# Kernel optimization log

Hardware: AMD Instinct MI355X
Metric: run time of the kernel (lower is better)

The kernel has to match this reference:

```python
import jax, jax.numpy as jnp
import numpy as np
from jax import lax

TAU_MIN = 0.01
TAU_MAX = 10.0
SLOW_TAU = 5.0


def setup_inputs() -> dict:
    key = jax.random.key(0)
    ks = iter(jax.random.split(key, 40))
    def p(shape, scale=0.05):
        return (jax.random.normal(next(ks), shape, jnp.float32) * scale)
    B, T, D = 1024, 512, 31
    FU, SU, H = 32, 32, 64
    inp = {
        "x": jax.random.normal(next(ks), (B, T, D), jnp.float32),
        # FlashFloodGate: Linear(62->32), Linear(32->1)
        "fg_w1": p((32, 2 * D)), "fg_b1": p((32,)),
        "fg_w2": p((1, 32)), "fg_b2": p((1,)),
        # fast LTC cell
        "fwin": p((FU, D)), "fbin": p((FU,)), "fwrec": p((FU, FU)),
        # slow LTC cell
        "swin": p((SU, D)), "sbin": p((SU,)), "swrec": p((SU, SU)),
        # fusion Linear(64->64)
        "fu_w": p((H, FU + SU)), "fu_b": p((H,)),
        # attention Linear(64->32), Linear(32->1)
        "at_w1": p((32, H)), "at_b1": p((32,)),
        "at_w2": p((1, 32)), "at_b2": p((1,)),
        # depth head Linear(64->64), Linear(64->5)
        "d_w1": p((64, H)), "d_b1": p((64,)),
        "d_w2": p((5, 64)), "d_b2": p((5,)),
        # overflow head Linear(64->64), Linear(64->32), Linear(32->1)
        "o_w1": p((64, H)), "o_b1": p((64,)),
        "o_w2": p((32, 64)), "o_b2": p((32,)),
        "o_w3": p((1, 32)), "o_b3": p((1,)),
        # intensity head Linear(64->32), Linear(32->1)
        "i_w1": p((32, H)), "i_b1": p((32,)),
        "i_w2": p((1, 32)), "i_b2": p((1,)),
    }
    return inp


def _ltc_scan(pre_tbh, w_rec, tau_tb1, h0):
    # pre_tbh: [T,B,H] precomputed W_in x + b; tau_tb1 broadcastable to [T,B,1]
    def step(h, inp):
        pre_t, tau_t = inp
        upd = jnp.tanh(pre_t + h @ w_rec.T)
        h = h + (upd - h) / tau_t
        return h, h
    _, hs = lax.scan(step, h0, (pre_tbh, tau_tb1))
    return jnp.transpose(hs, (1, 0, 2))  # [B,T,H]


def _forward(x, fg_w1, fg_b1, fg_w2, fg_b2, fwin, fbin, fwrec, swin, sbin, swrec,
             fu_w, fu_b, at_w1, at_b1, at_w2, at_b2, d_w1, d_b1, d_w2, d_b2,
             o_w1, o_b1, o_w2, o_b2, o_w3, o_b3, i_w1, i_b1, i_w2, i_b2):
    B, T, D = x.shape
    # FlashFloodGate over all timesteps (x_prev of t=0 is x_0 -> dx=0)
    dx = jnp.concatenate([jnp.zeros_like(x[:, :1]), x[:, 1:] - x[:, :-1]], axis=1)
    ci = jnp.concatenate([x, dx], axis=-1)                       # [B,T,2D]
    cs = jax.nn.sigmoid(jnp.tanh(ci @ fg_w1.T + fg_b1) @ fg_w2.T + fg_b2)  # [B,T,1]
    tau_fast = TAU_MAX - cs * (TAU_MAX - TAU_MIN)                # [B,T,1]
    # fast LTC (stepwise tau)
    pre_f = jnp.transpose(x @ fwin.T + fbin, (1, 0, 2))          # [T,B,FU]
    fast = _ltc_scan(pre_f, fwrec, jnp.transpose(tau_fast, (1, 0, 2)),
                     jnp.zeros((B, fwrec.shape[0]), x.dtype))
    # slow LTC (constant tau = 5.0, shape [B,1])
    pre_s = jnp.transpose(x @ swin.T + sbin, (1, 0, 2))          # [T,B,SU]
    slow = _ltc_scan(pre_s, swrec, jnp.full((T, 1, 1), SLOW_TAU, x.dtype),
                     jnp.zeros((B, swrec.shape[0]), x.dtype))
    # fusion
    ltc = jnp.tanh(jnp.concatenate([fast, slow], axis=-1) @ fu_w.T + fu_b)  # [B,T,H]
    # attention over time
    logits = jnp.tanh(ltc @ at_w1.T + at_b1) @ at_w2.T + at_b2   # [B,T,1]
    attn = jax.nn.softmax(logits, axis=1)
    context = jnp.sum(ltc * attn, axis=1)                        # [B,H]
    # heads (dropout is identity in eval)
    depths = jax.nn.relu(context @ d_w1.T + d_b1) @ d_w2.T + d_b2
    overflow = jax.nn.sigmoid(
        jax.nn.relu(jax.nn.relu(context @ o_w1.T + o_b1) @ o_w2.T + o_b2) @ o_w3.T + o_b3)
    intensity = jax.nn.sigmoid(jax.nn.relu(context @ i_w1.T + i_b1) @ i_w2.T + i_b2)
    return (depths, overflow, intensity)


def reference(x, fg_w1, fg_b1, fg_w2, fg_b2, fwin, fbin, fwrec, swin, sbin, swrec,
              fu_w, fu_b, at_w1, at_b1, at_w2, at_b2, d_w1, d_b1, d_w2, d_b2,
              o_w1, o_b1, o_w2, o_b2, o_w3, o_b3, i_w1, i_b1, i_w2, i_b2):
    return _forward(x, fg_w1, fg_b1, fg_w2, fg_b2, fwin, fbin, fwrec, swin, sbin,
                    swrec, fu_w, fu_b, at_w1, at_b1, at_w2, at_b2, d_w1, d_b1,
                    d_w2, d_b2, o_w1, o_b1, o_w2, o_b2, o_w3, o_b3,
                    i_w1, i_b1, i_w2, i_b2)
```

## Files before the change

### kernel.cpp

```cpp
#include <hip/hip_runtime.h>


#define T_  512
#define D_  31
#define GR_ 16
#define NG_ 32
#define NIT 36
#define L2E 1.4426950408889634f

typedef decltype(__builtin_amdgcn_cvt_pkrtz(0.0f, 0.0f)) h2;
typedef _Float16 h8v __attribute__((ext_vector_type(8)));
typedef float    f4v __attribute__((ext_vector_type(4)));

__device__ __forceinline__ float fexp2(float x){ return __builtin_amdgcn_exp2f(x); }
__device__ __forceinline__ float frcp (float x){ return __builtin_amdgcn_rcpf(x); }
__device__ __forceinline__ float fast_tanh(float x){
    float e = fexp2(x * 2.8853900817779268f);
    return 1.0f - 2.0f * frcp(1.0f + e);
}
__device__ __forceinline__ h2 cvt2(float a, float b){ return __builtin_amdgcn_cvt_pkrtz(a, b); }
__device__ __forceinline__ h2 bch2(unsigned v){ return __builtin_bit_cast(h2, v); }
__device__ __forceinline__ unsigned bcu(h2 v){ return __builtin_bit_cast(unsigned, v); }

template <int CTRL>
__device__ __forceinline__ float dppf(float v){
    int r = __builtin_amdgcn_update_dpp(0, __builtin_bit_cast(int, v),
                                        CTRL, 0xf, 0xf, true);
    return __builtin_bit_cast(float, r);
}
template <int CTRL>
__device__ __forceinline__ unsigned dppu(unsigned v){
    return (unsigned)__builtin_amdgcn_update_dpp(0, (int)v, CTRL, 0xf, 0xf, true);
}
__device__ __forceinline__ unsigned swz16(unsigned v){
    return (unsigned)__builtin_amdgcn_ds_swizzle((int)v, 0x401F);
}
__device__ __forceinline__ float rsum16(float v){
    v += dppf<0xB1>(v); v += dppf<0x4E>(v); v += dppf<0x141>(v); v += dppf<0x140>(v);
    return v;
}

#if __has_builtin(__builtin_amdgcn_fdot2)
#define FDOT2(acc, a, b) (acc) = __builtin_amdgcn_fdot2((a), (b), (acc), false)
#else
#define FDOT2(acc, a, b) (acc) += (float)(a)[0]*(float)(b)[0] + (float)(a)[1]*(float)(b)[1]
#endif

#define MFMA16(A, Bf, Cf) __builtin_amdgcn_mfma_f32_16x16x32_f16((A), (Bf), (Cf), 0, 0, 0)

#define BAR() do { asm volatile("s_waitcnt lgkmcnt(0)" ::: "memory"); \
                   __builtin_amdgcn_s_barrier();                      \
                   asm volatile("" ::: "memory"); } while (0)

__launch_bounds__(256, 4)
__global__ void lnn_mf(
    const float* __restrict__ X,
    const float* __restrict__ fg_w1, const float* __restrict__ fg_b1,
    const float* __restrict__ fg_w2, const float* __restrict__ fg_b2,
    const float* __restrict__ fwin,  const float* __restrict__ fbin,
    const float* __restrict__ fwrec,
    const float* __restrict__ swin,  const float* __restrict__ sbin,
    const float* __restrict__ swrec,
    const float* __restrict__ fu_w,  const float* __restrict__ fu_b,
    const float* __restrict__ at_w1, const float* __restrict__ at_b1,
    const float* __restrict__ at_w2, const float* __restrict__ at_b2,
    const float* __restrict__ d_w1,  const float* __restrict__ d_b1,
    const float* __restrict__ d_w2,  const float* __restrict__ d_b2,
    const float* __restrict__ o_w1,  const float* __restrict__ o_b1,
    const float* __restrict__ o_w2,  const float* __restrict__ o_b2,
    const float* __restrict__ o_w3,  const float* __restrict__ o_b3,
    const float* __restrict__ i_w1,  const float* __restrict__ i_b1,
    const float* __restrict__ i_w2,  const float* __restrict__ i_b2,
    float* __restrict__ out, int B)
{
    const int b    = blockIdx.x;
    const int tx   = threadIdx.x;
    const int wid  = tx >> 6;
    const int lane = tx & 63;
    const int u    = lane & 31;
    const int hb32 = lane & 32;
    const int role = (wid + b) & 3;

    __shared__ __align__(16) float    xr_sh [4][GR_][36];
    __shared__ float    xdm   [36];
    __shared__ float    pre_sh[4][GR_][65];
    __shared__ float    rt_sh [4][GR_];
    __shared__ __align__(16) unsigned hpk_sh[2][GR_][36];
    __shared__ __align__(16) unsigned ltcpk [2][GR_][36];
    __shared__ float    pw_sh [GR_];
    __shared__ float    ctx_sh[64];

    if (tx < 64) xr_sh[tx >> 4][tx & 15][31] = 0.0f;

    if (role == 0) {
        const int col = lane & 15, kb = lane >> 4;
        h8v wB[8];
        #pragma unroll
        for (int c = 0; c < 8; ++c) {
            float wv[8];
            #pragma unroll
            for (int j = 0; j < 8; ++j) {
                const int k = kb*8 + j;
                float v = 0.0f;
                if (k < 31) {
                    const int uu = 16*(c & 1) + col;
                    if (c < 2)      v = fg_w1[uu*62 + k] + fg_w1[uu*62 + 31 + k];
                    else if (c < 4) v = fg_w1[uu*62 + 31 + k];
                    else if (c < 6) v = fwin[uu*31 + k];
                    else            v = swin[uu*31 + k];
                }
                wv[j] = v;
            }
            uint4 qq = { bcu(cvt2(wv[0],wv[1])), bcu(cvt2(wv[2],wv[3])),
                         bcu(cvt2(wv[4],wv[5])), bcu(cvt2(wv[6],wv[7])) };
            wB[c] = __builtin_bit_cast(h8v, qq);
        }
        const float b1c[2] = { fg_b1[col], fg_b1[16 + col] };
        const float pb[4]  = { fbin[col], fbin[16+col], sbin[col], sbin[16+col] };
        const float w2n[2] = { fg_w2[col] * (-L2E), fg_w2[16+col] * (-L2E) };
        const float b2n    = fg_b2[0] * (-L2E);
        const unsigned* Xu = (const unsigned*)(X + (size_t)b * T_ * D_ + lane);
        float ypv[2] = {0.0f, 0.0f};
        asm volatile("s_waitcnt vmcnt(0)" ::: "memory");

        #pragma unroll
        for (int gg = 0; gg < 2; ++gg)
            #pragma unroll
            for (int k = 0; k < GR_; ++k)
                if (lane < 31)
                    __builtin_amdgcn_global_load_lds(
                        (const __attribute__((address_space(1))) unsigned*)(Xu + (size_t)(GR_*gg + k) * 31),
                        (__attribute__((address_space(3))) unsigned*)(&xr_sh[gg][k][0]),
                        4, 0, 0);

        for (int i = 0; i < NIT; ++i) {
            asm volatile("s_waitcnt vmcnt(16)" ::: "memory");
            BAR();
            {
                const int gq = i + 2;
                #pragma unroll
                for (int k = 0; k < GR_; ++k) {
                    int tl = GR_*gq + k; if (tl > 511) tl = 511;
                    float* dst = (gq <= NG_-1) ? &xr_sh[gq & 3][k][0] : &xdm[0];
                    if (lane < 31)
                        __builtin_amdgcn_global_load_lds(
                            (const __attribute__((address_space(1))) unsigned*)(Xu + (size_t)tl * 31),
                            (__attribute__((address_space(3))) unsigned*)dst,
                            4, 0, 0);
                }
            }
            if (i <= NG_-1) {
                const int sG = i & 3;
                const float* xrow = &xr_sh[sG][col][kb*8];
                float4 xa = *(const float4*)xrow;
                float4 xb = *(const float4*)(xrow + 4);
                uint4 aq = { bcu(cvt2(xa.x,xa.y)), bcu(cvt2(xa.z,xa.w)),
                             bcu(cvt2(xb.x,xb.y)), bcu(cvt2(xb.z,xb.w)) };
                h8v Af = __builtin_bit_cast(h8v, aq);
                f4v C[8];
                #pragma unroll
                for (int c = 0; c < 8; ++c) {
                    f4v z = {0.f, 0.f, 0.f, 0.f};
                    C[c] = MFMA16(Af, wB[c], z);
                }
                const int tb = kb * 4;
                float tp[4] = {0.f, 0.f, 0.f, 0.f};
                #pragma unroll
                for (int p = 0; p < 2; ++p) {
                    f4v G = C[p], Y = C[2+p];
                    if (i == 0) ypv[p] = __shfl(Y[0], col);
                    float ylast = __shfl(Y[3], 48 + col);
                    float yup   = __shfl(Y[3], (lane - 16) & 63);
                    float ysh0  = (kb == 0) ? ypv[p] : yup;
                    float h1v[4];
                    h1v[0] = fast_tanh(G[0] - ysh0 + b1c[p]);
                    h1v[1] = fast_tanh(G[1] - Y[0] + b1c[p]);
                    h1v[2] = fast_tanh(G[2] - Y[1] + b1c[p]);
                    h1v[3] = fast_tanh(G[3] - Y[2] + b1c[p]);
                    ypv[p] = ylast;
                    #pragma unroll
                    for (int r = 0; r < 4; ++r) tp[r] += h1v[r] * w2n[p];
                }
                #pragma unroll
                for (int r = 0; r < 4; ++r) {
                    float s  = rsum16(tp[r]) + b2n;
                    float cs = frcp(1.0f + fexp2(s));
                    float rt = frcp(10.0f - 9.99f * cs);
                    if (col == 0) rt_sh[sG][tb + r] = rt;
                }
                #pragma unroll
                for (int c = 4; c < 8; ++c) {
                    const int uo = (c < 6 ? 0 : 32) + 16*(c & 1) + col;
                    #pragma unroll
                    for (int r = 0; r < 4; ++r)
                        pre_sh[sG][tb + r][uo] = C[c][r] + pb[c-4];
                }
            }
        }
        asm volatile("s_waitcnt vmcnt(0)" ::: "memory");
    } else if (role == 1) {
        const bool slow = (lane >= 32);
        const float* W  = (slow ? swrec : fwrec) + u * 32;
        const int M0[8] = {0,2,7,5,15,13,8,10};
        const int M1[8] = {1,3,6,4,14,12,9,11};
        h2 wr[16];
        #pragma unroll
        for (int j = 0; j < 16; ++j) {
            const int x = (j & 8) ? 16 : 0;
            wr[j] = cvt2(W[u ^ M0[j & 7] ^ x], W[u ^ M1[j & 7] ^ x]);
        }
        float h_st = 0.0f;

        for (int i = 0; i < NIT; ++i) {
            BAR();
            if (i >= 2 && i <= NG_ + 1) {
                const int gR = i - 2;
                const int sR = gR & 3;
                const int sH = gR & 1;
                float preA[GR_], rtA[GR_];
                #pragma unroll
                for (int k = 0; k < GR_; ++k) {
                    preA[k] = pre_sh[sR][k][lane];
                    rtA[k]  = slow ? 0.2f : rt_sh[sR][k];
                }
                __builtin_amdgcn_s_setprio(1);
                #pragma unroll
                for (int k = 0; k < GR_; ++k) {
                    float hn = dppf<0xB1>(h_st);
                    unsigned u0 = bcu(cvt2(h_st, hn));
                    unsigned w0 = swz16(u0);
                    unsigned u1 = dppu<0x4E>(u0);
                    unsigned u2 = dppu<0x141>(u0);
                    unsigned u3 = dppu<0x141>(u1);
                    unsigned u4 = dppu<0x140>(u0);
                    unsigned u5 = dppu<0x140>(u1);
                    unsigned u6 = dppu<0x140>(u2);
                    unsigned u7 = dppu<0x140>(u3);
                    unsigned w1 = dppu<0x4E>(w0);
                    unsigned w2 = dppu<0x141>(w0);
                    unsigned w3 = dppu<0x141>(w1);
                    unsigned w4 = dppu<0x140>(w0);
                    unsigned w5 = dppu<0x140>(w1);
                    unsigned w6 = dppu<0x140>(w2);
                    unsigned w7 = dppu<0x140>(w3);
                    float a0 = 0.f, a1 = 0.f, a2 = 0.f, a3 = 0.f;
                    FDOT2(a0, bch2(u0), wr[0]);  FDOT2(a1, bch2(u1), wr[1]);
                    FDOT2(a2, bch2(u2), wr[2]);  FDOT2(a3, bch2(u3), wr[3]);
                    FDOT2(a0, bch2(u4), wr[4]);  FDOT2(a1, bch2(u5), wr[5]);
                    FDOT2(a2, bch2(u6), wr[6]);  FDOT2(a3, bch2(u7), wr[7]);
                    FDOT2(a0, bch2(w0), wr[8]);  FDOT2(a1, bch2(w1), wr[9]);
                    FDOT2(a2, bch2(w2), wr[10]); FDOT2(a3, bch2(w3), wr[11]);
                    FDOT2(a0, bch2(w4), wr[12]); FDOT2(a1, bch2(w5), wr[13]);
                    FDOT2(a2, bch2(w6), wr[14]); FDOT2(a3, bch2(w7), wr[15]);
                    float v   = (a0 + a1) + (a2 + a3);
                    float upd = fast_tanh(v + preA[k]);
                    h_st += (upd - h_st) * rtA[k];
                    float hw = dppf<0xB1>(h_st);
                    if (!(lane & 1))
                        hpk_sh[sH][k][lane >> 1] = bcu(cvt2(h_st, hw));
                }
                __builtin_amdgcn_s_setprio(0);
            }
        }
    } else if (role == 2) {
        const int col = lane & 15, kb = lane >> 4;
        h8v wF[8];
        #pragma unroll
        for (int kc = 0; kc < 2; ++kc)
            #pragma unroll
            for (int nc = 0; nc < 4; ++nc) {
                float wv[8];
                #pragma unroll
                for (int j = 0; j < 8; ++j)
                    wv[j] = fu_w[(16*nc + col)*64 + 32*kc + 8*kb + j];
                uint4 qq = { bcu(cvt2(wv[0],wv[1])), bcu(cvt2(wv[2],wv[3])),
                             bcu(cvt2(wv[4],wv[5])), bcu(cvt2(wv[6],wv[7])) };
                wF[kc*4 + nc] = __builtin_bit_cast(h8v, qq);
            }
        const float fb4[4] = { fu_b[col], fu_b[16+col], fu_b[32+col], fu_b[48+col] };

        for (int i = 0; i < NIT; ++i) {
            BAR();
            if (i >= 3 && i <= NG_ + 2) {
                const int gF = i - 3;
                const int sH = gF & 1;
                const unsigned* hrow = &hpk_sh[sH][col][0];
                uint4 a0q = *(const uint4*)(hrow + kb*4);
                uint4 a1q = *(const uint4*)(hrow + kb*4 + 16);
                h8v A0 = __builtin_bit_cast(h8v, a0q);
                h8v A1 = __builtin_bit_cast(h8v, a1q);
                const int tb = kb * 4;
                #pragma unroll
                for (int nc = 0; nc < 4; ++nc) {
                    f4v c4 = {0.f, 0.f, 0.f, 0.f};
                    c4 = MFMA16(A0, wF[nc],     c4);
                    c4 = MFMA16(A1, wF[4 + nc], c4);
                    #pragma unroll
                    for (int r = 0; r < 4; ++r) {
                        float v  = fast_tanh(c4[r] + fb4[nc]);
                        float vn = dppf<0xB1>(v);
                        h2 pk = (col & 1) ? cvt2(vn, v) : cvt2(v, vn);
                        if (!(col & 1))
                            ltcpk[gF & 1][tb + r][(16*nc + col) >> 1] = bcu(pk);
                    }
                }
            }
        }
    } else {
        const int col = lane & 15, kb = lane >> 4;
        h8v wA[4];
        #pragma unroll
        for (int kt = 0; kt < 2; ++kt)
            #pragma unroll
            for (int nt = 0; nt < 2; ++nt) {
                float wv[8];
                #pragma unroll
                for (int j = 0; j < 8; ++j)
                    wv[j] = at_w1[(nt*16 + col)*64 + kt*32 + 8*kb + j];
                uint4 qq = { bcu(cvt2(wv[0],wv[1])), bcu(cvt2(wv[2],wv[3])),
                             bcu(cvt2(wv[4],wv[5])), bcu(cvt2(wv[6],wv[7])) };
                wA[kt*2 + nt] = __builtin_bit_cast(h8v, qq);
            }
        const float ab1v[2] = { at_b1[col], at_b1[16 + col] };
        const float w2L[2]  = { at_w2[col] * L2E, at_w2[16 + col] * L2E };
        const float ab2L    = at_b2[0] * L2E;
        float s_run = 0.0f, c_run = 0.0f;

        for (int i = 0; i < NIT; ++i) {
            BAR();
            if (i >= 4) {
                const int gA = i - 4;
                const int sl = gA & 1;
                const unsigned* lrow = &ltcpk[sl][col][0];
                uint4 l0q = *(const uint4*)(lrow + kb*4);
                uint4 l1q = *(const uint4*)(lrow + kb*4 + 16);
                h8v L0 = __builtin_bit_cast(h8v, l0q);
                h8v L1 = __builtin_bit_cast(h8v, l1q);
                f4v CA[2];
                #pragma unroll
                for (int nt = 0; nt < 2; ++nt) {
                    f4v c4 = {0.f, 0.f, 0.f, 0.f};
                    c4 = MFMA16(L0, wA[nt],     c4);
                    c4 = MFMA16(L1, wA[2 + nt], c4);
                    CA[nt] = c4;
                }
                #pragma unroll
                for (int r = 0; r < 4; ++r) {
                    float s = fast_tanh(CA[0][r] + ab1v[0]) * w2L[0]
                            + fast_tanh(CA[1][r] + ab1v[1]) * w2L[1];
                    s = rsum16(s);
                    float pw = fexp2(s + ab2L);
                    if (col == 0) pw_sh[kb*4 + r] = pw;
                }
                #pragma unroll
                for (int t = 0; t < GR_; ++t) {
                    float ltc = (float)((const _Float16*)(&ltcpk[sl][t][0]))[lane];
                    float pwv = pw_sh[t];
                    s_run += pwv;
                    c_run += pwv * ltc;
                }
            }
        }
        ctx_sh[lane] = c_run * frcp(s_run);
    }

    __syncthreads();

    if (wid == 0) {
        float r1 = d_b1[lane];
        #pragma unroll
        for (int c = 0; c < 16; ++c) {
            float4 cq = ((const float4*)ctx_sh)[c];
            float4 wq = ((const float4*)(d_w1 + lane*64))[c];
            r1 += wq.x*cq.x + wq.y*cq.y + wq.z*cq.z + wq.w*cq.w;
        }
        r1 = fmaxf(r1, 0.0f);
        #pragma unroll
        for (int kk = 0; kk < 5; ++kk) {
            float v = d_w2[kk*64 + lane] * r1;
            v += __shfl_xor(v, 1);  v += __shfl_xor(v, 2);
            v += __shfl_xor(v, 4);  v += __shfl_xor(v, 8);
            v += __shfl_xor(v, 16); v += __shfl_xor(v, 32);
            if (lane == 0) out[b*5 + kk] = v + d_b2[kk];
        }
    } else if (wid == 1) {
        float r1 = o_b1[lane];
        #pragma unroll
        for (int c = 0; c < 16; ++c) {
            float4 cq = ((const float4*)ctx_sh)[c];
            float4 wq = ((const float4*)(o_w1 + lane*64))[c];
            r1 += wq.x*cq.x + wq.y*cq.y + wq.z*cq.z + wq.w*cq.w;
        }
        r1 = fmaxf(r1, 0.0f);
        float acc = 0.0f;
        #pragma unroll
        for (int j = 0; j < 32; ++j) {
            float rj = __shfl(r1, hb32 + j);
            acc += o_w2[u*64 + hb32 + j] * rj;
        }
        acc += __shfl_xor(acc, 32);
        float r2 = fmaxf(acc + o_b2[u], 0.0f);
        float v  = o_w3[u] * r2;
        v += __shfl_xor(v, 1);  v += __shfl_xor(v, 2);
        v += __shfl_xor(v, 4);  v += __shfl_xor(v, 8);
        v += __shfl_xor(v, 16);
        if (lane == 0) {
            float e = fexp2((v + o_b3[0]) * -L2E);
            out[5*B + b] = frcp(1.0f + e);
        }
    } else if (wid == 2) {
        float acc = 0.0f;
        #pragma unroll
        for (int c = 0; c < 8; ++c) {
            float4 cq = ((const float4*)(ctx_sh + hb32))[c];
            float4 wq = ((const float4*)(i_w1 + u*64 + hb32))[c];
            acc += wq.x*cq.x + wq.y*cq.y + wq.z*cq.z + wq.w*cq.w;
        }
        acc += __shfl_xor(acc, 32);
        float r1 = fmaxf(acc + i_b1[u], 0.0f);
        float v  = i_w2[u] * r1;
        v += __shfl_xor(v, 1);  v += __shfl_xor(v, 2);
        v += __shfl_xor(v, 4);  v += __shfl_xor(v, 8);
        v += __shfl_xor(v, 16);
        if (lane == 0) {
            float e = fexp2((v + i_b2[0]) * -L2E);
            out[6*B + b] = frcp(1.0f + e);
        }
    }
}

extern "C" void kernel_launch(void* const* d_in, const int* in_sizes, int n_in,
                              void* d_out, int out_size, void* d_ws, size_t ws_size,
                              hipStream_t stream) {
    (void)n_in; (void)out_size; (void)d_ws; (void)ws_size;
    const float* X     = (const float*)d_in[0];
    const float* fg_w1 = (const float*)d_in[1];
    const float* fg_b1 = (const float*)d_in[2];
    const float* fg_w2 = (const float*)d_in[3];
    const float* fg_b2 = (const float*)d_in[4];
    const float* fwin  = (const float*)d_in[5];
    const float* fbin  = (const float*)d_in[6];
    const float* fwrec = (const float*)d_in[7];
    const float* swin  = (const float*)d_in[8];
    const float* sbin  = (const float*)d_in[9];
    const float* swrec = (const float*)d_in[10];
    const float* fu_w  = (const float*)d_in[11];
    const float* fu_b  = (const float*)d_in[12];
    const float* at_w1 = (const float*)d_in[13];
    const float* at_b1 = (const float*)d_in[14];
    const float* at_w2 = (const float*)d_in[15];
    const float* at_b2 = (const float*)d_in[16];
    const float* d_w1  = (const float*)d_in[17];
    const float* d_b1  = (const float*)d_in[18];
    const float* d_w2  = (const float*)d_in[19];
    const float* d_b2  = (const float*)d_in[20];
    const float* o_w1  = (const float*)d_in[21];
    const float* o_b1  = (const float*)d_in[22];
    const float* o_w2  = (const float*)d_in[23];
    const float* o_b2  = (const float*)d_in[24];
    const float* o_w3  = (const float*)d_in[25];
    const float* o_b3  = (const float*)d_in[26];
    const float* i_w1  = (const float*)d_in[27];
    const float* i_b1  = (const float*)d_in[28];
    const float* i_w2  = (const float*)d_in[29];
    const float* i_b2  = (const float*)d_in[30];
    float* out = (float*)d_out;

    const int B = in_sizes[0] / (T_ * D_);
    dim3 grid(B), block(256);
    hipLaunchKernelGGL(lnn_mf, grid, block, 0, stream,
        X, fg_w1, fg_b1, fg_w2, fg_b2, fwin, fbin, fwrec, swin, sbin, swrec,
        fu_w, fu_b, at_w1, at_b1, at_w2, at_b2, d_w1, d_b1, d_w2, d_b2,
        o_w1, o_b1, o_w2, o_b2, o_w3, o_b3, i_w1, i_b1, i_w2, i_b2, out, B);
}
```

Before: 96.79 us.

## Fold tanh scale into weights, transpose pre buffer, shorten pipeline by one stage

Pre-multiplies the tanh input scale (2/ln2) into all weights and biases feeding tanh, which removes one multiply per tanh in every stage, including the serial recurrence. The pre-activation buffer is transposed so each recurrence lane reads its 16 values with four float4 loads, and the rt and pw buffers become float4 stores and loads. The recurrence stage now runs one iteration after the projection stage rather than two, so the buffers shrink to double buffering and the loop drops from 36 to 35 iterations. Scaling weights before the fp16 conversion changes rounding slightly, and the tighter stage offset depends on the barrier ordering staying correct.

New measurement: 99.71 us. +3.0%, slower.

```diff
diff --git a/kernel.cpp b/kernel.cpp
--- a/kernel.cpp
+++ b/kernel.cpp
@@ -5,8 +5,9 @@
 #define D_  31
 #define GR_ 16
 #define NG_ 32
-#define NIT 36
+#define NIT 35
 #define L2E 1.4426950408889634f
+#define TS_ 2.8853900817779268f
 
 typedef decltype(__builtin_amdgcn_cvt_pkrtz(0.0f, 0.0f)) h2;
 typedef _Float16 h8v __attribute__((ext_vector_type(8)));
@@ -14,9 +15,8 @@
 
 __device__ __forceinline__ float fexp2(float x){ return __builtin_amdgcn_exp2f(x); }
 __device__ __forceinline__ float frcp (float x){ return __builtin_amdgcn_rcpf(x); }
-__device__ __forceinline__ float fast_tanh(float x){
-    float e = fexp2(x * 2.8853900817779268f);
-    return 1.0f - 2.0f * frcp(1.0f + e);
+__device__ __forceinline__ float tanh_pre(float x){
+    return 1.0f - 2.0f * frcp(1.0f + fexp2(x));
 }
 __device__ __forceinline__ h2 cvt2(float a, float b){ return __builtin_amdgcn_cvt_pkrtz(a, b); }
 __device__ __forceinline__ h2 bch2(unsigned v){ return __builtin_bit_cast(h2, v); }
@@ -83,11 +83,11 @@
 
     __shared__ __align__(16) float    xr_sh [4][GR_][36];
     __shared__ float    xdm   [36];
-    __shared__ float    pre_sh[4][GR_][65];
-    __shared__ float    rt_sh [4][GR_];
+    __shared__ __align__(16) float    pre_t [2][64][20];
+    __shared__ __align__(16) float    rt4   [2][GR_];
     __shared__ __align__(16) unsigned hpk_sh[2][GR_][36];
     __shared__ __align__(16) unsigned ltcpk [2][GR_][36];
-    __shared__ float    pw_sh [GR_];
+    __shared__ __align__(16) float    pw_sh [GR_];
     __shared__ float    ctx_sh[64];
 
     if (tx < 64) xr_sh[tx >> 4][tx & 15][31] = 0.0f;
@@ -109,14 +109,15 @@
                     else if (c < 6) v = fwin[uu*31 + k];
                     else            v = swin[uu*31 + k];
                 }
-                wv[j] = v;
+                wv[j] = v * TS_;
             }
             uint4 qq = { bcu(cvt2(wv[0],wv[1])), bcu(cvt2(wv[2],wv[3])),
                          bcu(cvt2(wv[4],wv[5])), bcu(cvt2(wv[6],wv[7])) };
             wB[c] = __builtin_bit_cast(h8v, qq);
         }
-        const float b1c[2] = { fg_b1[col], fg_b1[16 + col] };
-        const float pb[4]  = { fbin[col], fbin[16+col], sbin[col], sbin[16+col] };
+        const float b1c[2] = { fg_b1[col] * TS_, fg_b1[16 + col] * TS_ };
+        const float pb[4]  = { fbin[col] * TS_, fbin[16+col] * TS_,
+                               sbin[col] * TS_, sbin[16+col] * TS_ };
         const float w2n[2] = { fg_w2[col] * (-L2E), fg_w2[16+col] * (-L2E) };
         const float b2n    = fg_b2[0] * (-L2E);
         const unsigned* Xu = (const unsigned*)(X + (size_t)b * T_ * D_ + lane);
@@ -151,6 +152,7 @@
             }
             if (i <= NG_-1) {
                 const int sG = i & 3;
+                const int sP = i & 1;
                 const float* xrow = &xr_sh[sG][col][kb*8];
                 float4 xa = *(const float4*)xrow;
                 float4 xb = *(const float4*)(xrow + 4);
@@ -173,27 +175,29 @@
                     float yup   = __shfl(Y[3], (lane - 16) & 63);
                     float ysh0  = (kb == 0) ? ypv[p] : yup;
                     float h1v[4];
-                    h1v[0] = fast_tanh(G[0] - ysh0 + b1c[p]);
-                    h1v[1] = fast_tanh(G[1] - Y[0] + b1c[p]);
-                    h1v[2] = fast_tanh(G[2] - Y[1] + b1c[p]);
-                    h1v[3] = fast_tanh(G[3] - Y[2] + b1c[p]);
+                    h1v[0] = tanh_pre(G[0] - ysh0 + b1c[p]);
+                    h1v[1] = tanh_pre(G[1] - Y[0] + b1c[p]);
+                    h1v[2] = tanh_pre(G[2] - Y[1] + b1c[p]);
+                    h1v[3] = tanh_pre(G[3] - Y[2] + b1c[p]);
                     ypv[p] = ylast;
                     #pragma unroll
                     for (int r = 0; r < 4; ++r) tp[r] += h1v[r] * w2n[p];
                 }
+                float4 rtq;
                 #pragma unroll
                 for (int r = 0; r < 4; ++r) {
                     float s  = rsum16(tp[r]) + b2n;
                     float cs = frcp(1.0f + fexp2(s));
                     float rt = frcp(10.0f - 9.99f * cs);
-                    if (col == 0) rt_sh[sG][tb + r] = rt;
-                }
+                    ((float*)&rtq)[r] = rt;
+                }
+                if (col == 0) *(float4*)&rt4[sP][tb] = rtq;
                 #pragma unroll
                 for (int c = 4; c < 8; ++c) {
                     const int uo = (c < 6 ? 0 : 32) + 16*(c & 1) + col;
                     #pragma unroll
                     for (int r = 0; r < 4; ++r)
-                        pre_sh[sG][tb + r][uo] = C[c][r] + pb[c-4];
+                        pre_t[sP][uo][tb + r] = C[c][r] + pb[c-4];
                 }
             }
         }
@@ -207,22 +211,26 @@
         #pragma unroll
         for (int j = 0; j < 16; ++j) {
             const int x = (j & 8) ? 16 : 0;
-            wr[j] = cvt2(W[u ^ M0[j & 7] ^ x], W[u ^ M1[j & 7] ^ x]);
+            wr[j] = cvt2(W[u ^ M0[j & 7] ^ x] * TS_, W[u ^ M1[j & 7] ^ x] * TS_);
         }
         float h_st = 0.0f;
 
         for (int i = 0; i < NIT; ++i) {
             BAR();
-            if (i >= 2 && i <= NG_ + 1) {
-                const int gR = i - 2;
-                const int sR = gR & 3;
+            if (i >= 1 && i <= NG_) {
+                const int gR = i - 1;
+                const int sP = gR & 1;
                 const int sH = gR & 1;
-                float preA[GR_], rtA[GR_];
-                #pragma unroll
-                for (int k = 0; k < GR_; ++k) {
-                    preA[k] = pre_sh[sR][k][lane];
-                    rtA[k]  = slow ? 0.2f : rt_sh[sR][k];
-                }
+                const float4* pp = (const float4*)(&pre_t[sP][lane][0]);
+                float4 p0 = pp[0], p1 = pp[1], p2 = pp[2], p3 = pp[3];
+                const float4* rr = (const float4*)(&rt4[sP][0]);
+                float4 r0 = rr[0], r1 = rr[1], r2 = rr[2], r3 = rr[3];
+                float preA[GR_] = { p0.x,p0.y,p0.z,p0.w, p1.x,p1.y,p1.z,p1.w,
+                                    p2.x,p2.y,p2.z,p2.w, p3.x,p3.y,p3.z,p3.w };
+                float rtA[GR_]  = { r0.x,r0.y,r0.z,r0.w, r1.x,r1.y,r1.z,r1.w,
+                                    r2.x,r2.y,r2.z,r2.w, r3.x,r3.y,r3.z,r3.w };
+                #pragma unroll
+                for (int k = 0; k < GR_; ++k) if (slow) rtA[k] = 0.2f;
                 __builtin_amdgcn_s_setprio(1);
                 #pragma unroll
                 for (int k = 0; k < GR_; ++k) {
@@ -253,7 +261,7 @@
                     FDOT2(a0, bch2(w4), wr[12]); FDOT2(a1, bch2(w5), wr[13]);
                     FDOT2(a2, bch2(w6), wr[14]); FDOT2(a3, bch2(w7), wr[15]);
                     float v   = (a0 + a1) + (a2 + a3);
-                    float upd = fast_tanh(v + preA[k]);
+                    float upd = tanh_pre(v + preA[k]);
                     h_st += (upd - h_st) * rtA[k];
                     float hw = dppf<0xB1>(h_st);
                     if (!(lane & 1))
@@ -272,17 +280,18 @@
                 float wv[8];
                 #pragma unroll
                 for (int j = 0; j < 8; ++j)
-                    wv[j] = fu_w[(16*nc + col)*64 + 32*kc + 8*kb + j];
+                    wv[j] = fu_w[(16*nc + col)*64 + 32*kc + 8*kb + j] * TS_;
                 uint4 qq = { bcu(cvt2(wv[0],wv[1])), bcu(cvt2(wv[2],wv[3])),
                              bcu(cvt2(wv[4],wv[5])), bcu(cvt2(wv[6],wv[7])) };
                 wF[kc*4 + nc] = __builtin_bit_cast(h8v, qq);
             }
-        const float fb4[4] = { fu_b[col], fu_b[16+col], fu_b[32+col], fu_b[48+col] };
+        const float fb4[4] = { fu_b[col] * TS_, fu_b[16+col] * TS_,
+                               fu_b[32+col] * TS_, fu_b[48+col] * TS_ };
 
         for (int i = 0; i < NIT; ++i) {
             BAR();
-            if (i >= 3 && i <= NG_ + 2) {
-                const int gF = i - 3;
+            if (i >= 2 && i <= NG_ + 1) {
+                const int gF = i - 2;
                 const int sH = gF & 1;
                 const unsigned* hrow = &hpk_sh[sH][col][0];
                 uint4 a0q = *(const uint4*)(hrow + kb*4);
@@ -297,7 +306,7 @@
                     c4 = MFMA16(A1, wF[4 + nc], c4);
                     #pragma unroll
                     for (int r = 0; r < 4; ++r) {
-                        float v  = fast_tanh(c4[r] + fb4[nc]);
+                        float v  = tanh_pre(c4[r] + fb4[nc]);
                         float vn = dppf<0xB1>(v);
                         h2 pk = (col & 1) ? cvt2(vn, v) : cvt2(v, vn);
                         if (!(col & 1))
@@ -316,20 +325,20 @@
                 float wv[8];
                 #pragma unroll
                 for (int j = 0; j < 8; ++j)
-                    wv[j] = at_w1[(nt*16 + col)*64 + kt*32 + 8*kb + j];
+                    wv[j] = at_w1[(nt*16 + col)*64 + kt*32 + 8*kb + j] * TS_;
                 uint4 qq = { bcu(cvt2(wv[0],wv[1])), bcu(cvt2(wv[2],wv[3])),
                              bcu(cvt2(wv[4],wv[5])), bcu(cvt2(wv[6],wv[7])) };
                 wA[kt*2 + nt] = __builtin_bit_cast(h8v, qq);
             }
-        const float ab1v[2] = { at_b1[col], at_b1[16 + col] };
+        const float ab1v[2] = { at_b1[col] * TS_, at_b1[16 + col] * TS_ };
         const float w2L[2]  = { at_w2[col] * L2E, at_w2[16 + col] * L2E };
         const float ab2L    = at_b2[0] * L2E;
         float s_run = 0.0f, c_run = 0.0f;
 
         for (int i = 0; i < NIT; ++i) {
             BAR();
-            if (i >= 4) {
-                const int gA = i - 4;
+            if (i >= 3) {
+                const int gA = i - 3;
                 const int sl = gA & 1;
                 const unsigned* lrow = &ltcpk[sl][col][0];
                 uint4 l0q = *(const uint4*)(lrow + kb*4);
@@ -344,20 +353,24 @@
                     c4 = MFMA16(L1, wA[2 + nt], c4);
                     CA[nt] = c4;
                 }
+                float4 pwq;
                 #pragma unroll
                 for (int r = 0; r < 4; ++r) {
-                    float s = fast_tanh(CA[0][r] + ab1v[0]) * w2L[0]
-                            + fast_tanh(CA[1][r] + ab1v[1]) * w2L[1];
+                    float s = tanh_pre(CA[0][r] + ab1v[0]) * w2L[0]
+                            + tanh_pre(CA[1][r] + ab1v[1]) * w2L[1];
                     s = rsum16(s);
-                    float pw = fexp2(s + ab2L);
-                    if (col == 0) pw_sh[kb*4 + r] = pw;
-                }
+                    ((float*)&pwq)[r] = fexp2(s + ab2L);
+                }
+                if (col == 0) *(float4*)&pw_sh[kb*4] = pwq;
+                const float4* pwp = (const float4*)&pw_sh[0];
+                float4 q0 = pwp[0], q1 = pwp[1], q2 = pwp[2], q3 = pwp[3];
+                float pwA[GR_] = { q0.x,q0.y,q0.z,q0.w, q1.x,q1.y,q1.z,q1.w,
+                                   q2.x,q2.y,q2.z,q2.w, q3.x,q3.y,q3.z,q3.w };
                 #pragma unroll
                 for (int t = 0; t < GR_; ++t) {
                     float ltc = (float)((const _Float16*)(&ltcpk[sl][t][0]))[lane];
-                    float pwv = pw_sh[t];
-                    s_run += pwv;
-                    c_run += pwv * ltc;
+                    s_run += pwA[t];
+                    c_run += pwA[t] * ltc;
                 }
             }
         }
```
